# Kernel optimization log

Hardware: AMD Instinct MI355X
Metric: run time of the kernel (lower is better)

## Reference

```python
import jax, jax.numpy as jnp
import numpy as np

P = 17  # prediction chunk size
H = 50  # hidden size

def _lstm_cell(x, h, c, Wih, Whh, bih, bhh):
    # torch LSTMCell: gates = x@Wih^T + bih + h@Whh^T + bhh, order i,f,g,o
    g = x @ Wih.T + h @ Whh.T + (bih + bhh)
    i, f, gg, o = jnp.split(g, 4, axis=-1)
    c_new = jax.nn.sigmoid(f) * c + jax.nn.sigmoid(i) * jnp.tanh(gg)
    h_new = jax.nn.sigmoid(o) * jnp.tanh(c_new)
    return h_new, c_new

def setup_inputs() -> dict:
    key = jax.random.key(0)
    ks = jax.random.split(key, 16)
    B, T = 2048, 512
    s = 1.0 / np.sqrt(H)
    u = lambda k, shp: jax.random.uniform(k, shp, jnp.float32, -s, s)
    return {
        "x": jax.random.normal(ks[0], (B, T * P), jnp.float32),
        "W_ih1": u(ks[1], (4 * H, P)),  "W_hh1": u(ks[2], (4 * H, H)),
        "b_ih1": u(ks[3], (4 * H,)),    "b_hh1": u(ks[4], (4 * H,)),
        "W_ih2": u(ks[5], (4 * H, H)),  "W_hh2": u(ks[6], (4 * H, H)),
        "b_ih2": u(ks[7], (4 * H,)),    "b_hh2": u(ks[8], (4 * H,)),
        "W_ih3": u(ks[9], (4 * H, H)),  "W_hh3": u(ks[10], (4 * H, H)),
        "b_ih3": u(ks[11], (4 * H,)),   "b_hh3": u(ks[12], (4 * H,)),
        "W_lin": u(ks[13], (P, H)),     "b_lin": u(ks[14], (P,)),
        "future": 544,
    }

def reference(x, W_ih1, W_hh1, b_ih1, b_hh1, W_ih2, W_hh2, b_ih2, b_hh2,
              W_ih3, W_hh3, b_ih3, b_hh3, W_lin, b_lin, future):
    B = x.shape[0]
    T = x.shape[1] // P
    xs = x.reshape(B, T, P).transpose(1, 0, 2)  # [T, B, P]
    z = jnp.zeros((B, H), jnp.float32)
    init = (z, z, z, z, z, z)

    def cell_stack(state, inp):
        h1, c1, h2, c2, h3, c3 = state
        h1, c1 = _lstm_cell(inp, h1, c1, W_ih1, W_hh1, b_ih1, b_hh1)
        h2, c2 = _lstm_cell(h1, h2, c2, W_ih2, W_hh2, b_ih2, b_hh2)
        h3, c3 = _lstm_cell(h2, h3, c3, W_ih3, W_hh3, b_ih3, b_hh3)
        out = h3 @ W_lin.T + b_lin  # [B, P]
        return (h1, c1, h2, c2, h3, c3), out

    def step(state, xt):
        return cell_stack(state, xt)

    state, outs = jax.lax.scan(step, init, xs)  # outs: [T, B, P]

    n_future = int(future) // P
    if n_future > 0:
        last = outs[-1]

        def fstep(carry, _):
            state, out = carry
            state, out = cell_stack(state, out)
            return (state, out), out

        _, fouts = jax.lax.scan(fstep, (state, last), None, length=n_future)
        outs = jnp.concatenate([outs, fouts], axis=0)  # [T+next, B, P]

    return outs.transpose(1, 0, 2).reshape(B, -1)  # [B, (T+next)*P]
```

## Files before the change

### kernel.cpp

```cpp
#include <hip/hip_runtime.h>
#include <math.h>


#define BATCH    2048
#define PP       17
#define HH       50
#define GG       200
#define MROWS    8
#define NQ       5
#define NTHREADS 1024
#define NBLOCKS  (BATCH / MROWS)
#define TQ1      14
#define TQ2      20
#define TQ3      20

__device__ __forceinline__ float bf2f(unsigned short u) {
    unsigned int i = ((unsigned int)u) << 16;
    float f; __builtin_memcpy(&f, &i, 4); return f;
}
__device__ __forceinline__ unsigned short f2bf(float f) {
    unsigned int i; __builtin_memcpy(&i, &f, 4);
    return (unsigned short)((i + 0x7fffu + ((i >> 16) & 1u)) >> 16);
}
__device__ __forceinline__ float ldin(const void* p, long i, bool f32) {
    return f32 ? ((const float*)p)[i] : bf2f(((const unsigned short*)p)[i]);
}
__device__ __forceinline__ float fsig(float x) {
    float t = exp2f(-1.44269504089f * x);
    return __builtin_amdgcn_rcpf(1.0f + t);
}
__device__ __forceinline__ float ftanh(float x) {
    float t = exp2f(2.88539008178f * x);
    return 1.0f - 2.0f * __builtin_amdgcn_rcpf(t + 1.0f);
}

extern "C" __global__ void sniff_dtype(const unsigned short* __restrict__ w,
                                       int* __restrict__ flag) {
    int lane = threadIdx.x;
    bool bad = false;
#pragma unroll
    for (int t = 0; t < 4; ++t) {
        float v = bf2f(w[lane * 4 + t]);
        bad |= !(fabsf(v) <= 1.0f);
    }
    unsigned long long m = __ballot(bad);
    if (lane == 0) flag[0] = (m != 0ULL) ? 1 : 0;
}

template <int TQ>
__device__ __forceinline__ void gate_phase(const float* __restrict__ S,
                                           float* __restrict__ gb,
                                           const float w[TQ],
                                           int srow, int g, int q, bool active) {
    if (active) {
        float a[8] = {0, 0, 0, 0, 0, 0, 0, 0};
        const float4* Sp = (const float4*)(S + (srow + q * TQ) * MROWS);
#pragma unroll
        for (int t = 0; t < TQ; ++t) {
            float wv = w[t];
            float4 lo = Sp[2 * t];
            float4 hi = Sp[2 * t + 1];
            a[0] = fmaf(wv, lo.x, a[0]); a[1] = fmaf(wv, lo.y, a[1]);
            a[2] = fmaf(wv, lo.z, a[2]); a[3] = fmaf(wv, lo.w, a[3]);
            a[4] = fmaf(wv, hi.x, a[4]); a[5] = fmaf(wv, hi.y, a[5]);
            a[6] = fmaf(wv, hi.z, a[6]); a[7] = fmaf(wv, hi.w, a[7]);
        }
        float* d = gb + (q * MROWS) * GG + g;
#pragma unroll
        for (int m = 0; m < 8; ++m) d[m * GG] = a[m];
    }
}

__device__ __forceinline__ void lstm_update(float* __restrict__ S,
                                            const float* __restrict__ gb,
                                            const float* __restrict__ bs,
                                            float& c, int hrow, int tid) {
    int m = tid & 7;
    int j = tid >> 3;
    float ii = bs[j], ff = bs[50 + j], gg = bs[100 + j], oo = bs[150 + j];
#pragma unroll
    for (int q = 0; q < NQ; ++q) {
        const float* b = gb + (q * MROWS + m) * GG;
        ii += b[j]; ff += b[50 + j]; gg += b[100 + j]; oo += b[150 + j];
    }
    float cn = fsig(ff) * c + fsig(ii) * ftanh(gg);
    c = cn;
    S[(hrow + j) * MROWS + m] = fsig(oo) * ftanh(cn);
}

extern "C" __global__
__attribute__((amdgpu_flat_work_group_size(NTHREADS, NTHREADS)))
__attribute__((amdgpu_waves_per_eu(4, 4)))
void lstm_persistent(const void* __restrict__ x,
                const void* __restrict__ wih1, const void* __restrict__ whh1,
                const void* __restrict__ bih1, const void* __restrict__ bhh1,
                const void* __restrict__ wih2, const void* __restrict__ whh2,
                const void* __restrict__ bih2, const void* __restrict__ bhh2,
                const void* __restrict__ wih3, const void* __restrict__ whh3,
                const void* __restrict__ bih3, const void* __restrict__ bhh3,
                const void* __restrict__ wlin, const void* __restrict__ blin,
                void* __restrict__ out, const int* __restrict__ flag,
                int T, int steps)
{
    const int tid = threadIdx.x;
    __shared__ float S[167 * MROWS];
    __shared__ float gb[NQ * MROWS * GG];
    __shared__ float WLt[50 * PP];
    __shared__ float bs1[GG], bs2[GG], bs3[GG], bl[PP];

    const bool f32 = (flag[0] != 0);

    const int q = tid / GG;
    const int g = tid - q * GG;
    const bool active = (tid < NQ * GG);

    float w1[TQ1], w2[TQ2], w3[TQ3];
    if (active) {
#pragma unroll
        for (int t = 0; t < TQ1; ++t) {
            int k = q * TQ1 + t;
            w1[t] = (k < 17) ? ldin(wih1, (long)g * 17 + k, f32)
                  : (k < 67) ? ldin(whh1, (long)g * 50 + (k - 17), f32)
                             : 0.0f;
        }
#pragma unroll
        for (int t = 0; t < TQ2; ++t) {
            int k = q * TQ2 + t;
            w2[t] = (k < 50) ? ldin(wih2, (long)g * 50 + k, f32)
                             : ldin(whh2, (long)g * 50 + (k - 50), f32);
        }
#pragma unroll
        for (int t = 0; t < TQ3; ++t) {
            int k = q * TQ3 + t;
            w3[t] = (k < 50) ? ldin(wih3, (long)g * 50 + k, f32)
                             : ldin(whh3, (long)g * 50 + (k - 50), f32);
        }
    }

    if (tid < GG) {
        bs1[tid] = ldin(bih1, tid, f32) + ldin(bhh1, tid, f32);
        bs2[tid] = ldin(bih2, tid, f32) + ldin(bhh2, tid, f32);
        bs3[tid] = ldin(bih3, tid, f32) + ldin(bhh3, tid, f32);
    } else if (tid < GG + PP) {
        bl[tid - GG] = ldin(blin, tid - GG, f32);
    }
    for (int i = tid; i < 50 * PP; i += NTHREADS) {
        int k = i / PP, p = i - k * PP;
        WLt[i] = ldin(wlin, (long)p * 50 + k, f32);
    }
    for (int i = tid; i < 1200; i += NTHREADS) S[136 + i] = 0.0f;

    const long rowBase = (long)blockIdx.x * MROWS;
    const long xStride = (long)T * PP;
    if (tid < 136) {
        int m = tid / PP, p = tid - (tid / PP) * PP;
        S[p * MROWS + m] = ldin(x, (rowBase + m) * xStride + p, f32);
    }
    float c1 = 0.0f, c2 = 0.0f, c3 = 0.0f;
    __syncthreads();

    const long outStride = (long)steps * PP;
    for (int s = 0; s < steps; ++s) {
        gate_phase<TQ1>(S, gb, w1, 0, g, q, active);
        __syncthreads();
        if (tid < 400) lstm_update(S, gb, bs1, c1, 17, tid);
        __syncthreads();
        gate_phase<TQ2>(S, gb, w2, 17, g, q, active);
        __syncthreads();
        if (tid < 400) lstm_update(S, gb, bs2, c2, 67, tid);
        __syncthreads();
        gate_phase<TQ3>(S, gb, w3, 67, g, q, active);
        __syncthreads();
        if (tid < 400) lstm_update(S, gb, bs3, c3, 117, tid);
        __syncthreads();
        if (tid < 136) {
            int m = tid / PP, p = tid - (tid / PP) * PP;
            float acc = bl[p];
#pragma unroll
            for (int k = 0; k < 50; ++k)
                acc = fmaf(WLt[k * PP + p], S[(117 + k) * MROWS + m], acc);
            long oi = (rowBase + m) * outStride + (long)s * PP + p;
            if (f32) ((float*)out)[oi] = acc;
            else     ((unsigned short*)out)[oi] = f2bf(acc);
            if (s + 1 >= T && s + 1 < steps)
                S[p * MROWS + m] = acc;
        } else if (tid >= 256 && tid < 392) {
            int u = tid - 256;
            int m = u / PP, p = u - (u / PP) * PP;
            if (s + 1 < T)
                S[p * MROWS + m] = ldin(x, (rowBase + m) * xStride + (long)(s + 1) * PP + p, f32);
        }
        __syncthreads();
    }
}

extern "C" void kernel_launch(void* const* d_in, const int* in_sizes, int n_in,
                              void* d_out, int out_size, void* d_ws, size_t ws_size,
                              hipStream_t stream) {
    (void)ws_size; (void)n_in;
    int* flag = (int*)d_ws;

    const int T     = in_sizes[0] / (BATCH * PP);
    const int steps = out_size / (BATCH * PP);

    sniff_dtype<<<1, 64, 0, stream>>>((const unsigned short*)d_in[1], flag);

    lstm_persistent<<<NBLOCKS, NTHREADS, 0, stream>>>(
        d_in[0],
        d_in[1], d_in[2], d_in[3], d_in[4],
        d_in[5], d_in[6], d_in[7], d_in[8],
        d_in[9], d_in[10], d_in[11], d_in[12],
        d_in[13], d_in[14],
        d_out, flag, T, steps);
}
```

Measured before the change: 3.530 ms.

## Register-block four gates per thread and halve the workgroup to 512 threads

Each active thread now computes four adjacent gate columns for all 8 batch rows. Each float4 of hidden state read from LDS is therefore reused across four weights instead of one. The reduction dimension is split into 10 chunks instead of 5, so the workgroup shrinks to 512 threads and waves_per_eu drops to 2. Partial sums are written as float4 stores, and the FMAs are emitted as inline v_fmac_f32. In exchange, lstm_update must sum twice as many partials from LDS, the gb buffer doubles in size, and per-thread register pressure rises.

```diff
diff --git a/kernel.cpp b/kernel.cpp
--- a/kernel.cpp
+++ b/kernel.cpp
@@ -7,12 +7,13 @@
 #define HH       50
 #define GG       200
 #define MROWS    8
-#define NQ       5
-#define NTHREADS 1024
+#define NQ       10
+#define NTHREADS 512
+#define NACTIVE  500
 #define NBLOCKS  (BATCH / MROWS)
-#define TQ1      14
-#define TQ2      20
-#define TQ3      20
+#define TQ1      7
+#define TQ2      10
+#define TQ3      10
 
 __device__ __forceinline__ float bf2f(unsigned short u) {
     unsigned int i = ((unsigned int)u) << 16;
@@ -33,6 +34,8 @@
     float t = exp2f(2.88539008178f * x);
     return 1.0f - 2.0f * __builtin_amdgcn_rcpf(t + 1.0f);
 }
+
+#define FMAC(A, W, X) asm("v_fmac_f32 %0, %1, %2" : "+v"(A) : "v"(W), "v"(X))
 
 extern "C" __global__ void sniff_dtype(const unsigned short* __restrict__ w,
                                        int* __restrict__ flag) {
@@ -50,24 +53,29 @@
 template <int TQ>
 __device__ __forceinline__ void gate_phase(const float* __restrict__ S,
                                            float* __restrict__ gb,
-                                           const float w[TQ],
-                                           int srow, int g, int q, bool active) {
+                                           const float (&w)[4][TQ],
+                                           int srow, int g4, int q, bool active) {
     if (active) {
-        float a[8] = {0, 0, 0, 0, 0, 0, 0, 0};
+        float a[4][8] = {};
         const float4* Sp = (const float4*)(S + (srow + q * TQ) * MROWS);
 #pragma unroll
         for (int t = 0; t < TQ; ++t) {
-            float wv = w[t];
             float4 lo = Sp[2 * t];
             float4 hi = Sp[2 * t + 1];
-            a[0] = fmaf(wv, lo.x, a[0]); a[1] = fmaf(wv, lo.y, a[1]);
-            a[2] = fmaf(wv, lo.z, a[2]); a[3] = fmaf(wv, lo.w, a[3]);
-            a[4] = fmaf(wv, hi.x, a[4]); a[5] = fmaf(wv, hi.y, a[5]);
-            a[6] = fmaf(wv, hi.z, a[6]); a[7] = fmaf(wv, hi.w, a[7]);
-        }
-        float* d = gb + (q * MROWS) * GG + g;
-#pragma unroll
-        for (int m = 0; m < 8; ++m) d[m * GG] = a[m];
+#pragma unroll
+            for (int e = 0; e < 4; ++e) {
+                float wv = w[e][t];
+                FMAC(a[e][0], wv, lo.x); FMAC(a[e][1], wv, lo.y);
+                FMAC(a[e][2], wv, lo.z); FMAC(a[e][3], wv, lo.w);
+                FMAC(a[e][4], wv, hi.x); FMAC(a[e][5], wv, hi.y);
+                FMAC(a[e][6], wv, hi.z); FMAC(a[e][7], wv, hi.w);
+            }
+        }
+#pragma unroll
+        for (int m = 0; m < 8; ++m) {
+            float4 v; v.x = a[0][m]; v.y = a[1][m]; v.z = a[2][m]; v.w = a[3][m];
+            *(float4*)(gb + (q * MROWS + m) * GG + 4 * g4) = v;
+        }
     }
 }
 
@@ -90,7 +98,7 @@
 
 extern "C" __global__
 __attribute__((amdgpu_flat_work_group_size(NTHREADS, NTHREADS)))
-__attribute__((amdgpu_waves_per_eu(4, 4)))
+__attribute__((amdgpu_waves_per_eu(2, 2)))
 void lstm_persistent(const void* __restrict__ x,
                 const void* __restrict__ wih1, const void* __restrict__ whh1,
                 const void* __restrict__ bih1, const void* __restrict__ bhh1,
@@ -110,30 +118,34 @@
 
     const bool f32 = (flag[0] != 0);
 
-    const int q = tid / GG;
-    const int g = tid - q * GG;
-    const bool active = (tid < NQ * GG);
-
-    float w1[TQ1], w2[TQ2], w3[TQ3];
+    const int q  = tid / 50;
+    const int g4 = tid - q * 50;
+    const bool active = (tid < NACTIVE);
+
+    float w1[4][TQ1], w2[4][TQ2], w3[4][TQ3];
     if (active) {
 #pragma unroll
-        for (int t = 0; t < TQ1; ++t) {
-            int k = q * TQ1 + t;
-            w1[t] = (k < 17) ? ldin(wih1, (long)g * 17 + k, f32)
-                  : (k < 67) ? ldin(whh1, (long)g * 50 + (k - 17), f32)
-                             : 0.0f;
-        }
-#pragma unroll
-        for (int t = 0; t < TQ2; ++t) {
-            int k = q * TQ2 + t;
-            w2[t] = (k < 50) ? ldin(wih2, (long)g * 50 + k, f32)
-                             : ldin(whh2, (long)g * 50 + (k - 50), f32);
-        }
-#pragma unroll
-        for (int t = 0; t < TQ3; ++t) {
-            int k = q * TQ3 + t;
-            w3[t] = (k < 50) ? ldin(wih3, (long)g * 50 + k, f32)
-                             : ldin(whh3, (long)g * 50 + (k - 50), f32);
+        for (int e = 0; e < 4; ++e) {
+            const int g = 4 * g4 + e;
+#pragma unroll
+            for (int t = 0; t < TQ1; ++t) {
+                int k = q * TQ1 + t;
+                w1[e][t] = (k < 17) ? ldin(wih1, (long)g * 17 + k, f32)
+                         : (k < 67) ? ldin(whh1, (long)g * 50 + (k - 17), f32)
+                                    : 0.0f;
+            }
+#pragma unroll
+            for (int t = 0; t < TQ2; ++t) {
+                int k = q * TQ2 + t;
+                w2[e][t] = (k < 50) ? ldin(wih2, (long)g * 50 + k, f32)
+                                    : ldin(whh2, (long)g * 50 + (k - 50), f32);
+            }
+#pragma unroll
+            for (int t = 0; t < TQ3; ++t) {
+                int k = q * TQ3 + t;
+                w3[e][t] = (k < 50) ? ldin(wih3, (long)g * 50 + k, f32)
+                                    : ldin(whh3, (long)g * 50 + (k - 50), f32);
+            }
         }
     }
 
@@ -161,15 +173,15 @@
 
     const long outStride = (long)steps * PP;
     for (int s = 0; s < steps; ++s) {
-        gate_phase<TQ1>(S, gb, w1, 0, g, q, active);
+        gate_phase<TQ1>(S, gb, w1, 0, g4, q, active);
         __syncthreads();
         if (tid < 400) lstm_update(S, gb, bs1, c1, 17, tid);
         __syncthreads();
-        gate_phase<TQ2>(S, gb, w2, 17, g, q, active);
+        gate_phase<TQ2>(S, gb, w2, 17, g4, q, active);
         __syncthreads();
         if (tid < 400) lstm_update(S, gb, bs2, c2, 67, tid);
         __syncthreads();
-        gate_phase<TQ3>(S, gb, w3, 67, g, q, active);
+        gate_phase<TQ3>(S, gb, w3, 67, g4, q, active);
         __syncthreads();
         if (tid < 400) lstm_update(S, gb, bs3, c3, 117, tid);
         __syncthreads();
```

Measured after the change: 3.660 ms. 1.04x slower.
